# Kernel tuning notes

Measured on AMD Instinct MI355X. Metric: run time of the kernel, lower is better.

Reference implementation:

```python
import jax, jax.numpy as jnp
import numpy as np

H = 12  # num_heads


def rotate_half(x):
    x1, x2 = jnp.split(x, 2, axis=-1)
    return jnp.concatenate([-x2, x1], axis=-1)


def setup_inputs() -> dict:
    key = jax.random.key(0)
    ks = jax.random.split(key, 8)
    B, N, C = 4, 2048, 768
    num_special = 5
    Ns = N - num_special
    D = C // H
    x = jax.random.normal(ks[0], (B, N, C), dtype=jnp.float32)
    rope_cos = jax.random.uniform(ks[1], (Ns, D), dtype=jnp.float32)
    rope_sin = jax.random.uniform(ks[2], (Ns, D), dtype=jnp.float32)
    W_qkv = jax.random.normal(ks[3], (C, 3 * C), dtype=jnp.float32) * (C ** -0.5)
    b_qkv = jax.random.normal(ks[4], (3 * C,), dtype=jnp.float32) * 0.02
    W_proj = jax.random.normal(ks[5], (C, C), dtype=jnp.float32) * (C ** -0.5)
    b_proj = jax.random.normal(ks[6], (C,), dtype=jnp.float32) * 0.02
    return {"x": x, "rope_cos": rope_cos, "rope_sin": rope_sin,
            "W_qkv": W_qkv, "b_qkv": b_qkv, "W_proj": W_proj, "b_proj": b_proj,
            "num_special": num_special}


def reference(x, rope_cos, rope_sin, W_qkv, b_qkv, W_proj, b_proj, num_special):
    B, N, C = x.shape
    D = C // H
    scale = D ** -0.5
    qkv = (x @ W_qkv + b_qkv).reshape(B, N, 3, H, D)
    qkv = jnp.transpose(qkv, (2, 0, 3, 1, 4))  # [3, B, H, N, D]
    q, k, v = qkv[0], qkv[1], qkv[2]
    # partial RoPE: special tokens untouched, spatial tokens rotated
    q_spec, q_spat = q[:, :, :num_special], q[:, :, num_special:]
    k_spec, k_spat = k[:, :, :num_special], k[:, :, num_special:]
    q_spat = q_spat * rope_cos + rotate_half(q_spat) * rope_sin
    k_spat = k_spat * rope_cos + rotate_half(k_spat) * rope_sin
    q = jnp.concatenate([q_spec, q_spat], axis=2)
    k = jnp.concatenate([k_spec, k_spat], axis=2)
    attn = jnp.einsum('bhqd,bhkd->bhqk', q, k) * scale  # [B,H,N,N]
    attn = jax.nn.softmax(attn, axis=-1)
    out = jnp.einsum('bhqk,bhkd->bhqd', attn, v)  # [B,H,N,D]
    out = jnp.transpose(out, (0, 2, 1, 3)).reshape(B, N, C)
    return out @ W_proj + b_proj
```

## Files before the change

kernel.cpp:

```cpp
#include <hip/hip_runtime.h>
#include <stdint.h>

typedef unsigned short u16;
typedef __bf16 bf16x8 __attribute__((ext_vector_type(8)));
typedef short s16x4 __attribute__((ext_vector_type(4)));
typedef float f32x4 __attribute__((ext_vector_type(4)));

typedef __attribute__((address_space(1))) void gvoid_t;
typedef __attribute__((address_space(3))) void lvoid_t;

struct alignas(16) U128 { uint32_t x, y, z, w; };
struct alignas(16) F128 { float x, y, z, w; };
struct alignas(8)  U64v { uint32_t x, y; };

__device__ __forceinline__ void gld16(const u16* g, u16* lds) {
  __builtin_amdgcn_global_load_lds((gvoid_t*)const_cast<u16*>(g),
                                   (lvoid_t*)lds, 16, 0, 0);
}

__device__ __forceinline__ u16 f2bf(float f) {
  uint32_t u = __builtin_bit_cast(uint32_t, f);
  u += 0x7FFFu + ((u >> 16) & 1u);
  return (u16)(u >> 16);
}
__device__ __forceinline__ float bf2f(u16 h) {
  return __builtin_bit_cast(float, (uint32_t)h << 16);
}
__device__ __forceinline__ bf16x8 ldfrag(const u16* p) {
  U128 u = *reinterpret_cast<const U128*>(p);
  return __builtin_bit_cast(bf16x8, u);
}
__device__ __forceinline__ uint32_t pkbf(float a, float b) {
  uint32_t ua = __builtin_bit_cast(uint32_t, a) + 0x8000u;
  uint32_t ub = __builtin_bit_cast(uint32_t, b) + 0x8000u;
  return (ua >> 16) | (ub & 0xFFFF0000u);
}

__device__ __forceinline__ float EXP2(float x) { return __builtin_amdgcn_exp2f(x); }

__global__ void cvt_f32_bf16(const float* __restrict__ in, u16* __restrict__ out) {
  int i = (blockIdx.x * 256 + threadIdx.x) * 4;
  F128 v = *reinterpret_cast<const F128*>(in + i);
  U64v o;
  o.x = (uint32_t)f2bf(v.x) | ((uint32_t)f2bf(v.y) << 16);
  o.y = (uint32_t)f2bf(v.z) | ((uint32_t)f2bf(v.w) << 16);
  *reinterpret_cast<U64v*>(out + i) = o;
}

__global__ void transpose_cvt(const float* __restrict__ W, u16* __restrict__ Wt,
                              int K, int N) {
  __shared__ float T[32][33];
  const int n0 = blockIdx.x * 32, k0 = blockIdx.y * 32;
  const int tid = threadIdx.x;
#pragma unroll
  for (int i = 0; i < 4; ++i) {
    int e = i * 256 + tid, r = e >> 5, c = e & 31;
    T[r][c] = W[(size_t)(k0 + r) * N + n0 + c];
  }
  __syncthreads();
#pragma unroll
  for (int i = 0; i < 4; ++i) {
    int e = i * 256 + tid, r = e >> 5, c = e & 31;
    Wt[(size_t)(n0 + r) * K + k0 + c] = f2bf(T[c][r]);
  }
}

__global__ __launch_bounds__(256, 2)
void gemm_bt(const u16* __restrict__ A, const u16* __restrict__ Bt,
             const float* __restrict__ bias, float* __restrict__ C,
             int M, int N, int K) {
  __shared__ u16 As[128 * 32];
  __shared__ u16 Bs[128 * 32];
  const int tid = threadIdx.x;
  const int wave = tid >> 6, lane = tid & 63;
  const int quad = lane >> 4, l16 = lane & 15;
  const int m0 = blockIdx.y * 128, n0 = blockIdx.x * 128;
  const int wr = (wave & 1) * 64, wc = (wave >> 1) * 64;

  f32x4 acc[4][4];
#pragma unroll
  for (int i = 0; i < 4; ++i)
#pragma unroll
    for (int j = 0; j < 4; ++j) acc[i][j] = (f32x4){0.f, 0.f, 0.f, 0.f};

  for (int k0 = 0; k0 < K; k0 += 32) {
    __syncthreads();
#pragma unroll
    for (int j = 0; j < 2; ++j) {
      int c = (wave * 2 + j) * 64 + lane;
      int row = c >> 2, kq = c & 3;
      gld16(A + (size_t)(m0 + row) * K + k0 + kq * 8, &As[(wave * 2 + j) * 512]);
      gld16(Bt + (size_t)(n0 + row) * K + k0 + kq * 8, &Bs[(wave * 2 + j) * 512]);
    }
    __syncthreads();
    bf16x8 af[4], bfr[4];
#pragma unroll
    for (int rb = 0; rb < 4; ++rb) af[rb] = ldfrag(&As[(wr + rb * 16 + l16) * 32 + quad * 8]);
#pragma unroll
    for (int cb = 0; cb < 4; ++cb) bfr[cb] = ldfrag(&Bs[(wc + cb * 16 + l16) * 32 + quad * 8]);
#pragma unroll
    for (int rb = 0; rb < 4; ++rb)
#pragma unroll
      for (int cb = 0; cb < 4; ++cb)
        acc[rb][cb] = __builtin_amdgcn_mfma_f32_16x16x32_bf16(af[rb], bfr[cb], acc[rb][cb], 0, 0, 0);
  }
#pragma unroll
  for (int cb = 0; cb < 4; ++cb) {
    int col = n0 + wc + cb * 16 + l16;
    float bv = bias[col];
#pragma unroll
    for (int rb = 0; rb < 4; ++rb) {
#pragma unroll
      for (int r = 0; r < 4; ++r) {
        int row = m0 + wr + rb * 16 + quad * 4 + r;
        C[(size_t)row * N + col] = acc[rb][cb][r] + bv;
      }
    }
  }
}

__global__ __launch_bounds__(256, 2)
void gemm_qkv_rope(const u16* __restrict__ A, const u16* __restrict__ Bt,
                   const float* __restrict__ bias,
                   const float* __restrict__ cosT, const float* __restrict__ sinT,
                   const int* __restrict__ nsp,
                   u16* __restrict__ Qo, u16* __restrict__ Ko, u16* __restrict__ Vto) {
  __shared__ u16 As[128 * 32];
  __shared__ u16 Bs[128 * 32];
  const int K = 768, N = 2304;
  const int tid = threadIdx.x;
  const int wave = tid >> 6, lane = tid & 63;
  const int quad = lane >> 4, l16 = lane & 15;
  const int m0 = blockIdx.y * 128, n0 = blockIdx.x * 128;
  const int wr = (wave & 1) * 64, wc = (wave >> 1) * 64;

  f32x4 acc[4][4];
#pragma unroll
  for (int i = 0; i < 4; ++i)
#pragma unroll
    for (int j = 0; j < 4; ++j) acc[i][j] = (f32x4){0.f, 0.f, 0.f, 0.f};

  for (int k0 = 0; k0 < K; k0 += 32) {
    __syncthreads();
#pragma unroll
    for (int j = 0; j < 2; ++j) {
      int c = (wave * 2 + j) * 64 + lane;
      int row = c >> 2, kq = c & 3;
      gld16(A + (size_t)(m0 + row) * K + k0 + kq * 8, &As[(wave * 2 + j) * 512]);
      gld16(Bt + (size_t)(n0 + row) * K + k0 + kq * 8, &Bs[(wave * 2 + j) * 512]);
    }
    __syncthreads();
    bf16x8 af[4], bfr[4];
#pragma unroll
    for (int rb = 0; rb < 4; ++rb) af[rb] = ldfrag(&As[(wr + rb * 16 + l16) * 32 + quad * 8]);
#pragma unroll
    for (int cb = 0; cb < 4; ++cb) bfr[cb] = ldfrag(&Bs[(wc + cb * 16 + l16) * 32 + quad * 8]);
#pragma unroll
    for (int rb = 0; rb < 4; ++rb)
#pragma unroll
      for (int cb = 0; cb < 4; ++cb)
        acc[rb][cb] = __builtin_amdgcn_mfma_f32_16x16x32_bf16(af[rb], bfr[cb], acc[rb][cb], 0, 0, 0);
  }

  const int sec = blockIdx.x / 6;
  const int gcol0 = n0 + wc;
  const int hh = (gcol0 >> 6) % 12;
  const int bb = m0 >> 11;
  const int nbase = m0 & 2047;
  const int bh = bb * 12 + hh;
  const int num_special = nsp[0];
  const float QS = 0.125f * 1.4426950408889634f;

  if (sec < 2) {
    u16* outp = sec ? Ko : Qo;
    const float qs = sec ? 1.0f : QS;
#pragma unroll
    for (int cbp = 0; cbp < 2; ++cbp) {
      const int d1 = cbp * 16 + l16;
      const int d2 = d1 + 32;
      const float bv1 = bias[gcol0 + d1];
      const float bv2 = bias[gcol0 + d2];
#pragma unroll
      for (int rb = 0; rb < 4; ++rb) {
#pragma unroll
        for (int r = 0; r < 4; ++r) {
          const int n = nbase + wr + rb * 16 + quad * 4 + r;
          float v1 = acc[rb][cbp][r] + bv1;
          float v2 = acc[rb][cbp + 2][r] + bv2;
          float o1, o2;
          if (n < num_special) {
            o1 = v1; o2 = v2;
          } else {
            int ns = n - num_special;
            float c1 = cosT[ns * 64 + d1], s1 = sinT[ns * 64 + d1];
            float c2 = cosT[ns * 64 + d2], s2 = sinT[ns * 64 + d2];
            o1 = v1 * c1 - v2 * s1;
            o2 = v2 * c2 + v1 * s2;
          }
          size_t ob = ((size_t)bh * 2048 + n) * 64;
          outp[ob + d1] = f2bf(o1 * qs);
          outp[ob + d2] = f2bf(o2 * qs);
        }
      }
    }
  } else {
#pragma unroll
    for (int cb = 0; cb < 4; ++cb) {
      const int d = cb * 16 + l16;
      const float bv = bias[gcol0 + d];
#pragma unroll
      for (int rb = 0; rb < 4; ++rb) {
        const int nr = nbase + wr + rb * 16 + quad * 4;
        U64v o;
        o.x = (uint32_t)f2bf(acc[rb][cb][0] + bv) |
              ((uint32_t)f2bf(acc[rb][cb][1] + bv) << 16);
        o.y = (uint32_t)f2bf(acc[rb][cb][2] + bv) |
              ((uint32_t)f2bf(acc[rb][cb][3] + bv) << 16);
        *(U64v*)&Vto[((size_t)bh * 64 + d) * 2048 + nr] = o;
      }
    }
  }
}

__global__ __launch_bounds__(256, 3)
void attn(const u16* __restrict__ Q, const u16* __restrict__ Kg,
          const u16* __restrict__ Vt, u16* __restrict__ Out) {
  __shared__ u16 smem[2 * 64 * 72];
  __shared__ float invS[64];
  u16* Ks = smem;
  u16* Vs = smem + 64 * 72;
  u16* Qs = smem;
  const int tid = threadIdx.x;
  const int wave = tid >> 6, lane = tid & 63;
  const int quad = lane >> 4, l16 = lane & 15;
  const int idx = blockIdx.x;
  const int bh = idx % 48, qt = idx / 48;
  const int b = bh / 12, h = bh % 12;
  const u16* Qb = Q + (size_t)bh * 2048 * 64;
  const u16* Kb = Kg + (size_t)bh * 2048 * 64;
  const u16* Vb = Vt + (size_t)bh * 64 * 2048;
  const int wkey0 = wave * 16;

#pragma unroll
  for (int j = 0; j < 2; ++j) {
    int c = j * 256 + tid;
    int row = c >> 3, kq = c & 7;
    *(U128*)&Qs[row * 72 + kq * 8] =
        *(const U128*)(Qb + (size_t)(qt * 64 + row) * 64 + kq * 8);
  }
  __syncthreads();
  bf16x8 qf[4][2];
#pragma unroll
  for (int m = 0; m < 4; ++m) {
    qf[m][0] = ldfrag(&Qs[(m * 16 + l16) * 72 + quad * 8]);
    qf[m][1] = ldfrag(&Qs[(m * 16 + l16) * 72 + quad * 8 + 32]);
  }

  f32x4 oacc[4][4];
#pragma unroll
  for (int m = 0; m < 4; ++m)
#pragma unroll
    for (int db = 0; db < 4; ++db) oacc[m][db] = (f32x4){0.f, 0.f, 0.f, 0.f};
  float psum[4] = {0.f, 0.f, 0.f, 0.f};

  for (int kt = 0; kt < 32; ++kt) {
    __syncthreads();
#pragma unroll
    for (int j = 0; j < 2; ++j) {
      int c = j * 256 + tid;
      int row = c >> 3, kq = c & 7;
      *(U128*)&Ks[row * 72 + kq * 8] =
          *(const U128*)(Kb + (size_t)(kt * 64 + row) * 64 + kq * 8);
      *(U128*)&Vs[row * 72 + kq * 8] =
          *(const U128*)(Vb + (size_t)row * 2048 + kt * 64 + kq * 8);
    }
    __syncthreads();

    bf16x8 ka0 = ldfrag(&Ks[(wkey0 + l16) * 72 + quad * 8]);
    bf16x8 ka1 = ldfrag(&Ks[(wkey0 + l16) * 72 + quad * 8 + 32]);

    s16x4 pf[4];
#pragma unroll
    for (int m = 0; m < 4; ++m) {
      f32x4 st = (f32x4){0.f, 0.f, 0.f, 0.f};
      st = __builtin_amdgcn_mfma_f32_16x16x32_bf16(ka0, qf[m][0], st, 0, 0, 0);
      st = __builtin_amdgcn_mfma_f32_16x16x32_bf16(ka1, qf[m][1], st, 0, 0, 0);
      float p0 = EXP2(st[0]);
      float p1 = EXP2(st[1]);
      float p2 = EXP2(st[2]);
      float p3 = EXP2(st[3]);
      psum[m] += (p0 + p1) + (p2 + p3);
      U64v pd;
      pd.x = pkbf(p0, p1);
      pd.y = pkbf(p2, p3);
      pf[m] = __builtin_bit_cast(s16x4, pd);
    }

#pragma unroll
    for (int db = 0; db < 4; ++db) {
      s16x4 vf = __builtin_bit_cast(s16x4,
          *(const U64v*)&Vs[(db * 16 + l16) * 72 + wkey0 + quad * 4]);
#pragma unroll
      for (int m = 0; m < 4; ++m)
        oacc[m][db] = __builtin_amdgcn_mfma_f32_16x16x16bf16_1k(pf[m], vf, oacc[m][db], 0, 0, 0);
    }
  }

#pragma unroll
  for (int m = 0; m < 4; ++m) {
    psum[m] += __shfl_xor(psum[m], 16, 64);
    psum[m] += __shfl_xor(psum[m], 32, 64);
  }
  __syncthreads();
  float* LS = (float*)smem;
  if (quad == 0) {
#pragma unroll
    for (int m = 0; m < 4; ++m) LS[wave * 64 + m * 16 + l16] = psum[m];
  }
  __syncthreads();
  if (tid < 64) {
    float tot = LS[tid] + LS[64 + tid] + LS[128 + tid] + LS[192 + tid];
    invS[tid] = 1.0f / tot;
  }

  float* OR = (float*)smem;
  const int q = tid >> 2;
  const int d0 = (tid & 3) * 4;
  const size_t obase = ((size_t)(b * 2048 + qt * 64 + q)) * 768 + h * 64 + d0;
#pragma unroll
  for (int db = 0; db < 4; ++db) {
    __syncthreads();
#pragma unroll
    for (int m = 0; m < 4; ++m)
#pragma unroll
      for (int r = 0; r < 4; ++r)
        OR[(wave * 64 + m * 16 + quad * 4 + r) * 18 + l16] = oacc[m][db][r];
    __syncthreads();
    float s0 = 0.f, s1 = 0.f, s2 = 0.f, s3 = 0.f;
#pragma unroll
    for (int w = 0; w < 4; ++w) {
      const float* p = &OR[(w * 64 + q) * 18 + d0];
      s0 += p[0]; s1 += p[1]; s2 += p[2]; s3 += p[3];
    }
    float iv = invS[q];
    U64v o;
    o.x = (uint32_t)f2bf(s0 * iv) | ((uint32_t)f2bf(s1 * iv) << 16);
    o.y = (uint32_t)f2bf(s2 * iv) | ((uint32_t)f2bf(s3 * iv) << 16);
    *(U64v*)&Out[obase + db * 16] = o;
  }
}

extern "C" void kernel_launch(void* const* d_in, const int* in_sizes, int n_in,
                              void* d_out, int out_size, void* d_ws, size_t ws_size,
                              hipStream_t stream) {
  (void)in_sizes; (void)n_in; (void)out_size; (void)ws_size;
  const float* x        = (const float*)d_in[0];
  const float* rope_cos = (const float*)d_in[1];
  const float* rope_sin = (const float*)d_in[2];
  const float* W_qkv    = (const float*)d_in[3];
  const float* b_qkv    = (const float*)d_in[4];
  const float* W_proj   = (const float*)d_in[5];
  const float* b_proj   = (const float*)d_in[6];
  const int*   nsp      = (const int*)d_in[7];
  float* out = (float*)d_out;

  char* ws = (char*)d_ws;
  u16* Xb   = (u16*)(ws);
  u16* Wqkt = (u16*)(ws + 12582912);
  u16* Wpt  = (u16*)(ws + 16121856);
  u16* Qb   = (u16*)(ws + 55050240);
  u16* Kb   = (u16*)(ws + 67633152);
  u16* Vtb  = (u16*)(ws + 80216064);
  u16* att  = (u16*)(ws + 92798976);

  cvt_f32_bf16<<<6144, 256, 0, stream>>>(x, Xb);
  transpose_cvt<<<dim3(72, 24), 256, 0, stream>>>(W_qkv, Wqkt, 768, 2304);
  transpose_cvt<<<dim3(24, 24), 256, 0, stream>>>(W_proj, Wpt, 768, 768);
  gemm_qkv_rope<<<dim3(18, 64), 256, 0, stream>>>(Xb, Wqkt, b_qkv, rope_cos, rope_sin,
                                                  nsp, Qb, Kb, Vtb);
  attn<<<1536, 256, 0, stream>>>(Qb, Kb, Vtb, att);
  gemm_bt<<<dim3(6, 64), 256, 0, stream>>>(att, Wpt, b_proj, out, 8192, 768, 768);
}
```

Before: 253.9 us.

## Load K/V fragments directly from global with register prefetch, drop LDS staging

The attention kernel stops staging K and V tiles through shared memory. Each wave now loads its own K and V fragments straight from global memory into registers, prefetching the next tile while computing the current one. This removes the two block-wide barriers per key tile and the LDS write/read traffic. In exchange it adds uncoalesced, narrow global loads (8-byte V reads strided by 2048) and more register pressure. The wave split is by key, so each wave only reads its own slice and no K/V data is reused across waves.

```diff
diff --git a/kernel.cpp b/kernel.cpp
--- a/kernel.cpp
+++ b/kernel.cpp
@@ -225,11 +225,8 @@
 __global__ __launch_bounds__(256, 3)
 void attn(const u16* __restrict__ Q, const u16* __restrict__ Kg,
           const u16* __restrict__ Vt, u16* __restrict__ Out) {
-  __shared__ u16 smem[2 * 64 * 72];
+  __shared__ float OR[4 * 64 * 18];
   __shared__ float invS[64];
-  u16* Ks = smem;
-  u16* Vs = smem + 64 * 72;
-  u16* Qs = smem;
   const int tid = threadIdx.x;
   const int wave = tid >> 6, lane = tid & 63;
   const int quad = lane >> 4, l16 = lane & 15;
@@ -241,19 +238,12 @@
   const u16* Vb = Vt + (size_t)bh * 64 * 2048;
   const int wkey0 = wave * 16;
 
-#pragma unroll
-  for (int j = 0; j < 2; ++j) {
-    int c = j * 256 + tid;
-    int row = c >> 3, kq = c & 7;
-    *(U128*)&Qs[row * 72 + kq * 8] =
-        *(const U128*)(Qb + (size_t)(qt * 64 + row) * 64 + kq * 8);
-  }
-  __syncthreads();
   bf16x8 qf[4][2];
 #pragma unroll
   for (int m = 0; m < 4; ++m) {
-    qf[m][0] = ldfrag(&Qs[(m * 16 + l16) * 72 + quad * 8]);
-    qf[m][1] = ldfrag(&Qs[(m * 16 + l16) * 72 + quad * 8 + 32]);
+    const u16* qp = Qb + (size_t)(qt * 64 + m * 16 + l16) * 64 + quad * 8;
+    qf[m][0] = ldfrag(qp);
+    qf[m][1] = ldfrag(qp + 32);
   }
 
   f32x4 oacc[4][4];
@@ -263,21 +253,24 @@
     for (int db = 0; db < 4; ++db) oacc[m][db] = (f32x4){0.f, 0.f, 0.f, 0.f};
   float psum[4] = {0.f, 0.f, 0.f, 0.f};
 
+  const u16* Kp = Kb + (size_t)(wkey0 + l16) * 64 + quad * 8;
+  const u16* Vp = Vb + (size_t)l16 * 2048 + wkey0 + quad * 4;
+
+  bf16x8 ka0 = ldfrag(Kp), ka1 = ldfrag(Kp + 32);
+  U64v vcur[4];
+#pragma unroll
+  for (int db = 0; db < 4; ++db)
+    vcur[db] = *(const U64v*)(Vp + (size_t)db * 16 * 2048);
+
   for (int kt = 0; kt < 32; ++kt) {
-    __syncthreads();
-#pragma unroll
-    for (int j = 0; j < 2; ++j) {
-      int c = j * 256 + tid;
-      int row = c >> 3, kq = c & 7;
-      *(U128*)&Ks[row * 72 + kq * 8] =
-          *(const U128*)(Kb + (size_t)(kt * 64 + row) * 64 + kq * 8);
-      *(U128*)&Vs[row * 72 + kq * 8] =
-          *(const U128*)(Vb + (size_t)row * 2048 + kt * 64 + kq * 8);
-    }
-    __syncthreads();
-
-    bf16x8 ka0 = ldfrag(&Ks[(wkey0 + l16) * 72 + quad * 8]);
-    bf16x8 ka1 = ldfrag(&Ks[(wkey0 + l16) * 72 + quad * 8 + 32]);
+    const int ktn = (kt + 1) & 31;
+    const u16* Kn = Kp + (size_t)ktn * 64 * 64;
+    const u16* Vn = Vp + (size_t)ktn * 64;
+    bf16x8 kn0 = ldfrag(Kn), kn1 = ldfrag(Kn + 32);
+    U64v vnxt[4];
+#pragma unroll
+    for (int db = 0; db < 4; ++db)
+      vnxt[db] = *(const U64v*)(Vn + (size_t)db * 16 * 2048);
 
     s16x4 pf[4];
 #pragma unroll
@@ -298,12 +291,15 @@
 
 #pragma unroll
     for (int db = 0; db < 4; ++db) {
-      s16x4 vf = __builtin_bit_cast(s16x4,
-          *(const U64v*)&Vs[(db * 16 + l16) * 72 + wkey0 + quad * 4]);
+      s16x4 vf = __builtin_bit_cast(s16x4, vcur[db]);
 #pragma unroll
       for (int m = 0; m < 4; ++m)
         oacc[m][db] = __builtin_amdgcn_mfma_f32_16x16x16bf16_1k(pf[m], vf, oacc[m][db], 0, 0, 0);
     }
+
+    ka0 = kn0; ka1 = kn1;
+#pragma unroll
+    for (int db = 0; db < 4; ++db) vcur[db] = vnxt[db];
   }
 
 #pragma unroll
@@ -312,7 +308,7 @@
     psum[m] += __shfl_xor(psum[m], 32, 64);
   }
   __syncthreads();
-  float* LS = (float*)smem;
+  float* LS = OR;
   if (quad == 0) {
 #pragma unroll
     for (int m = 0; m < 4; ++m) LS[wave * 64 + m * 16 + l16] = psum[m];
@@ -323,7 +319,6 @@
     invS[tid] = 1.0f / tot;
   }
 
-  float* OR = (float*)smem;
   const int q = tid >> 2;
   const int d0 = (tid & 3) * 4;
   const size_t obase = ((size_t)(b * 2048 + qt * 64 + q)) * 768 + h * 64 + d0;
```

New measurement: 317.5 us. 1.25x slower.
